# Optimization experiments

Hardware: AMD Instinct MI355X
Metric: run time of the kernel (lower is better)

The kernel has to match this reference:

```python
import jax, jax.numpy as jnp
import numpy as np

N = 32768   # nodes
E = 131072  # directed edges
B = 8       # graphs in batch
F_IN = 1025
NEG = -1e30
EPS = 1e-5


def _lin_init(k, i, o):
    k1, k2 = jax.random.split(k)
    s = 1.0 / np.sqrt(i)
    return (jax.random.uniform(k1, (i, o), jnp.float32, -s, s),
            jax.random.uniform(k2, (o,), jnp.float32, -s, s))


def _bn_init(k, c):
    k1, k2, k3, k4 = jax.random.split(k, 4)
    gamma = jax.random.uniform(k1, (c,), jnp.float32, 0.5, 1.5)
    beta = jax.random.normal(k2, (c,), jnp.float32) * 0.1
    mean = jax.random.normal(k3, (c,), jnp.float32) * 0.1
    var = jax.random.uniform(k4, (c,), jnp.float32, 0.5, 1.5)
    return jnp.stack([gamma, beta, mean, var])  # [4, c]


def setup_inputs() -> dict:
    key = jax.random.key(0)
    ks = jax.random.split(key, 16)
    x = jax.random.normal(ks[0], (N, F_IN), jnp.float32)
    edge_index = jax.random.randint(ks[1], (2, E), 0, N, dtype=jnp.int32)
    batch = jnp.sort(jax.random.randint(ks[2], (N,), 0, B, dtype=jnp.int32))
    pool_w, pool_b = _lin_init(ks[3], 2 * F_IN, 1)
    c1_w0, _ = _lin_init(ks[4], F_IN, 512)
    c1_w1, c1_b = _lin_init(ks[5], F_IN, 512)
    c2_w0, _ = _lin_init(ks[6], 512, 512)
    c2_w1, c2_b = _lin_init(ks[7], 512, 512)
    bn1 = _bn_init(ks[8], 512)
    bn2 = _bn_init(ks[9], 512)
    bn3 = _bn_init(ks[10], 512)
    bn4 = _bn_init(ks[11], 256)
    lin1_w, lin1_b = _lin_init(ks[12], 1024, 512)
    lin2_w, lin2_b = _lin_init(ks[13], 512, 256)
    lin3_w, lin3_b = _lin_init(ks[14], 256, 4)
    return dict(x=x, edge_index=edge_index, batch=batch,
                pool_w=pool_w, pool_b=pool_b,
                c1_w0=c1_w0, c1_w1=c1_w1, c1_b=c1_b,
                c2_w0=c2_w0, c2_w1=c2_w1, c2_b=c2_b,
                bn1=bn1, bn2=bn2, bn3=bn3, bn4=bn4,
                lin1_w=lin1_w, lin1_b=lin1_b,
                lin2_w=lin2_w, lin2_b=lin2_b,
                lin3_w=lin3_w, lin3_b=lin3_b)


def _batchnorm(h, p):
    g, b, m, v = p[0], p[1], p[2], p[3]
    return (h - m) * jax.lax.rsqrt(v + EPS) * g + b


def _cheb(h, row, col, w, w0, w1, b):
    # ChebConv K=2, sym norm, lambda_max=2: out = h@W0 + (L_hat h)@W1 + b,
    # L_hat = -D^{-1/2} A D^{-1/2} (self-loops removed, diag of scaled L is 0)
    deg = jax.ops.segment_sum(w, row, num_segments=N)
    dis = jnp.where(deg > 0, 1.0 / jnp.sqrt(jnp.maximum(deg, 1e-12)), 0.0)
    nrm = -w * dis[row] * dis[col]
    tx1 = jax.ops.segment_sum(nrm[:, None] * h[row], col, num_segments=N)
    return h @ w0 + tx1 @ w1 + b


def _forward(x, edge_index, batch, pool_w, pool_b,
             c1_w0, c1_w1, c1_b, c2_w0, c2_w1, c2_b,
             bn1, bn2, bn3, bn4,
             lin1_w, lin1_b, lin2_w, lin2_b, lin3_w, lin3_b):
    u, v = edge_index[0], edge_index[1]

    # ---- EdgePooling: edge scores = softmax over dst segments, +0.5 ----
    e = (jnp.concatenate([x[u], x[v]], axis=1) @ pool_w + pool_b)[:, 0]  # [E]
    m = jax.ops.segment_max(e, v, num_segments=N)
    ex = jnp.exp(e - m[v])
    score = ex / jax.ops.segment_sum(ex, v, num_segments=N)[v] + 0.5

    # ---- greedy maximal matching in descending score order ----
    order = jnp.argsort(-score)

    def step(used, k):
        uu, vv = u[k], v[k]
        ok = jnp.logical_not(used[uu] | used[vv])
        used = used.at[uu].set(used[uu] | ok)
        used = used.at[vv].set(used[vv] | ok)
        return used, ok

    _, ok_sorted = jax.lax.scan(step, jnp.zeros((N,), bool), order)
    sel = jnp.zeros((E,), bool).at[order].set(ok_sorted)

    rep = jnp.minimum(u, v)  # cluster representative of a merged edge
    cluster = jnp.arange(N, dtype=jnp.int32)
    cluster = cluster.at[jnp.where(sel, u, N)].set(rep, mode='drop')
    cluster = cluster.at[jnp.where(sel, v, N)].set(rep, mode='drop')
    node_score = jnp.ones((N,), x.dtype).at[jnp.where(sel, rep, N)].set(score, mode='drop')
    px = jnp.zeros_like(x).at[cluster].add(x) * node_score[:, None]  # pooled node feats
    valid = cluster == jnp.arange(N, dtype=jnp.int32)  # surviving cluster rows

    # ---- coarsened edge_index, coalesced (dedup), self-loops dropped ----
    cu, cv = cluster[u], cluster[v]
    nonloop = cu != cv
    key = jnp.where(nonloop, cu * N + cv, N * N + jnp.arange(E, dtype=jnp.int32))
    o2 = jnp.argsort(key)
    sk = key[o2]
    first = jnp.concatenate([jnp.ones((1,), bool), sk[1:] != sk[:-1]])
    keep_sorted = first & (sk < N * N)
    w = jnp.zeros((E,), x.dtype).at[o2].set(keep_sorted.astype(x.dtype))

    # ---- two ChebConv + BN(eval) + ReLU ----
    h = jax.nn.relu(_batchnorm(_cheb(px, cu, cv, w, c1_w0, c1_w1, c1_b), bn1))
    h = jax.nn.relu(_batchnorm(_cheb(h, cu, cv, w, c2_w0, c2_w1, c2_b), bn2))

    # ---- global max + mean pool over valid nodes per graph ----
    hmax = jax.ops.segment_max(jnp.where(valid[:, None], h, NEG), batch, num_segments=B)
    cnt = jax.ops.segment_sum(valid.astype(h.dtype), batch, num_segments=B)
    hmean = jax.ops.segment_sum(jnp.where(valid[:, None], h, 0.0), batch,
                                num_segments=B) / jnp.maximum(cnt, 1.0)[:, None]
    g = jnp.concatenate([hmax, hmean], axis=1)  # [B, 1024]

    # ---- readout MLP (dropout off in eval) ----
    g = jax.nn.relu(_batchnorm(g @ lin1_w + lin1_b, bn3))
    g = jax.nn.relu(_batchnorm(g @ lin2_w + lin2_b, bn4))
    feature = g
    out = jax.nn.log_softmax(jax.nn.relu(g @ lin3_w + lin3_b), axis=-1)
    return out, feature


def reference(x, edge_index, batch, pool_w, pool_b,
              c1_w0, c1_w1, c1_b, c2_w0, c2_w1, c2_b,
              bn1, bn2, bn3, bn4,
              lin1_w, lin1_b, lin2_w, lin2_b, lin3_w, lin3_b):
    return _forward(x, edge_index, batch, pool_w, pool_b,
                    c1_w0, c1_w1, c1_b, c2_w0, c2_w1, c2_b,
                    bn1, bn2, bn3, bn4,
                    lin1_w, lin1_b, lin2_w, lin2_b, lin3_w, lin3_b)
```

## Files before the change

kernel.cpp:

```cpp
#include <hip/hip_runtime.h>
#include <hip/hip_bf16.h>
#include <cstdint>
#include <cmath>

typedef unsigned int u32;
typedef unsigned long long u64;
typedef float f32x4 __attribute__((ext_vector_type(4)));
typedef __bf16 bf16x8 __attribute__((ext_vector_type(8)));
typedef unsigned short us8 __attribute__((ext_vector_type(8)));
typedef unsigned short us4 __attribute__((ext_vector_type(4)));

#define NN 32768
#define NE 131072
#define FIN 1025
#define HTS 262144
#define HTM (HTS - 1)

#define WS_A_D    0ul
#define WS_B_D    262144ul
#define WS_EMAX   524288ul
#define WS_SSUM   655360ul
#define WS_EXD    917504ul
#define WS_CIN    917504ul
#define WS_KEY    1966080ul
#define WS_BEST   3014656ul
#define WS_USED   3276800ul
#define WS_CUR    3276800ul
#define WS_ACT0   3407872ul
#define WS_ACT1   3932160ul
#define WS_BTHI   0ul
#define WS_BT2    3407872ul
#define WS_HT     1966080ul
#define WS_RACC1  2097152ul
#define WS_RACC2  2113536ul
#define WS_CIDX   2129920ul
#define WS_PERM   2260992ul
#define WS_BSUM   2392064ul
#define WS_BOFF   2393088ul
#define WS_SCORE  4456448ul
#define WS_CSRA   4456448ul
#define WS_SEL    4980736ul
#define WS_CSRC   4980736ul
#define WS_CLUST  5505024ul
#define WS_OTHER  5636096ul
#define WS_NSC    5767168ul
#define WS_CEU    5898240ul
#define WS_CEV    6422528ul
#define WS_DEG    6946816ul
#define WS_OFF    6946816ul
#define WS_DIS    7077888ul
#define WS_PXL    7077888ul
#define WS_MISC   7208960ul
#define WS_GMAX   7209216ul
#define WS_GSUM   7225600ul
#define WS_GCNT   7241984ul
#define WS_P      7242240ul
#define WS_PB     74351104ul
#define WS_H      141459968ul

__device__ __forceinline__ u32 enc_f(float f) {
    u32 b = __float_as_uint(f);
    return (b & 0x80000000u) ? ~b : (b | 0x80000000u);
}
__device__ __forceinline__ float dec_f(u32 m) {
    return (m & 0x80000000u) ? __uint_as_float(m ^ 0x80000000u) : __uint_as_float(~m);
}
__device__ __forceinline__ double wave_sum(double v) {
    #pragma unroll
    for (int off = 32; off > 0; off >>= 1) v += __shfl_down(v, off, 64);
    return v;
}
__device__ __forceinline__ unsigned short f2bf(float v) {
    u32 b = __float_as_uint(v);
    u32 r = b + 0x7FFFu + ((b >> 16) & 1u);
    return (unsigned short)(r >> 16);
}
__device__ __forceinline__ float bf2f(unsigned short h) {
    return __uint_as_float(((u32)h) << 16);
}
__device__ __forceinline__ bf16x8 ld_frag(const unsigned short* p) {
    union { us8 u; bf16x8 b; } t;
    t.u = *(const us8*)p;
    return t.b;
}
__device__ __forceinline__ void dma16(unsigned short* lds, const unsigned short* g) {
    __builtin_amdgcn_global_load_lds((const __attribute__((address_space(1))) u32*)g,
                                     (__attribute__((address_space(3))) u32*)lds, 16, 0, 0);
}

__global__ void node_dots(const float* __restrict__ x, const float* __restrict__ pw,
                          double* a_d, double* b_d,
                          u32* emax, double* ssum, u32* deg, int* misc,
                          u32* gmaxb, float* gsum, float* gcnt,
                          u64* best, u32* used, int* clus, int* other, float* nsc) {
    int gid = blockIdx.x * blockDim.x + threadIdx.x;
    if (gid < NN) {
        emax[gid] = 0u; ssum[gid] = 0.0; deg[gid] = 0u;
        best[gid] = ~0ull; used[gid] = 0u;
        clus[gid] = gid; other[gid] = -1; nsc[gid] = 1.0f;
    }
    if (gid < 4096) { gmaxb[gid] = 0u; gsum[gid] = 0.0f; }
    if (gid < 64) { misc[gid] = (gid == 1) ? NE : 0; gcnt[gid] = 0.0f; }

    int wave = gid >> 6;
    int lane = threadIdx.x & 63;
    if (wave >= NN) return;
    const float* xr = x + (size_t)wave * FIN;
    double s0 = 0.0, s1 = 0.0;
    for (int f = lane; f < FIN; f += 64) {
        double xv = (double)xr[f];
        s0 += xv * (double)pw[f];
        s1 += xv * (double)pw[FIN + f];
    }
    s0 = wave_sum(s0); s1 = wave_sum(s1);
    if (lane == 0) { a_d[wave] = s0; b_d[wave] = s1; }
}

__global__ void edge_p1(const int* __restrict__ ei, const double* __restrict__ a_d,
                        const double* __restrict__ b_d, const float* __restrict__ pb,
                        double* e_d, u32* emax) {
    int k = blockIdx.x * 256 + threadIdx.x;
    if (k >= NE) return;
    int u = ei[k], v = ei[NE + k];
    double e = a_d[u] + b_d[v] + (double)pb[0];
    e_d[k] = e;
    atomicMax(&emax[v], enc_f((float)e));
}
__global__ void edge_p2(const int* __restrict__ ei, double* e_d,
                        const u32* __restrict__ emax, double* ssum) {
    int k = blockIdx.x * 256 + threadIdx.x;
    if (k >= NE) return;
    int v = ei[NE + k];
    float mf = dec_f(emax[v]);
    double ex = exp(e_d[k] - (double)mf);
    e_d[k] = ex;
    unsafeAtomicAdd(&ssum[v], ex);
}
__global__ void edge_p3(const int* __restrict__ ei, const double* __restrict__ e_d,
                        const double* __restrict__ ssum, float* score, u64* key,
                        int* sel, int* act0, u64* best) {
    int k = blockIdx.x * 256 + threadIdx.x;
    if (k >= NE) return;
    int u = ei[k], v = ei[NE + k];
    float sc = (float)(e_d[k] / ssum[v] + 0.5);
    score[k] = sc;
    u32 m = enc_f(sc);
    u64 kk = ((u64)(m ^ 0xFFFFFFFFu) << 32) | (u32)k;
    key[k] = kk;
    sel[k] = 0;
    act0[k] = k;
    atomicMin(&best[u], kk);
    atomicMin(&best[v], kk);
}

__global__ void mk_sel(const u64* __restrict__ key, const int* __restrict__ ei,
                       const int* __restrict__ act, const int* __restrict__ cntp,
                       int* ncntp, const u64* __restrict__ best,
                       u32* used, int* sel) {
    int cnt = cntp[0];
    int stride = gridDim.x * blockDim.x;
    int gid = blockIdx.x * blockDim.x + threadIdx.x;
    if (gid == 0) ncntp[0] = 0;
    for (int i = gid; i < cnt; i += stride) {
        int e = act[i];
        u64 k = key[e];
        int a = ei[e], b = ei[NE + e];
        if (best[a] == k && best[b] == k) { sel[e] = 1; used[a] = 1u; used[b] = 1u; }
    }
}
__global__ void mk_compact(const int* __restrict__ ei, const int* __restrict__ act,
                           const int* __restrict__ cntp, int* nxt, int* ncntp,
                           u64* best, const u32* __restrict__ used) {
    int cnt = cntp[0];
    int stride = gridDim.x * blockDim.x;
    for (int i = blockIdx.x * blockDim.x + threadIdx.x; i < cnt; i += stride) {
        int e = act[i];
        int a = ei[e], b = ei[NE + e];
        best[a] = ~0ull; best[b] = ~0ull;
        bool live = !(used[a] | used[b]);
        u64 mask = __ballot(live);
        if (mask) {
            int lane = threadIdx.x & 63;
            int leader = __ffsll((unsigned long long)mask) - 1;
            int base = 0;
            if (lane == leader) base = atomicAdd(ncntp, __popcll(mask));
            base = __shfl(base, leader, 64);
            if (live) nxt[base + __popcll(mask & ((1ull << lane) - 1ull))] = e;
        }
    }
}
__global__ void mk_min(const u64* __restrict__ key, const int* __restrict__ ei,
                       const int* __restrict__ act, const int* __restrict__ cntp,
                       u64* best) {
    int cnt = cntp[0];
    int stride = gridDim.x * blockDim.x;
    for (int i = blockIdx.x * blockDim.x + threadIdx.x; i < cnt; i += stride) {
        int e = act[i];
        u64 k = key[e];
        atomicMin(&best[ei[e]], k);
        atomicMin(&best[ei[NE + e]], k);
    }
}
__global__ void __launch_bounds__(1024) match_fin(
        const u64* __restrict__ key, const int* __restrict__ ei,
        int* sel, u64* best, u32* used,
        int* listA, int* listB, const int* __restrict__ cntp) {
    int tid = threadIdx.x;
    int cnt = cntp[0];
    int* cur = listA; int* nxt = listB;
    __shared__ int s_n;
    for (int round = 0; round < 4096 && cnt > 0; ++round) {
        for (int i = tid; i < cnt; i += 1024) {
            int e = cur[i]; u64 k = key[e];
            atomicMin(&best[ei[e]], k);
            atomicMin(&best[ei[NE + e]], k);
        }
        __syncthreads();
        for (int i = tid; i < cnt; i += 1024) {
            int e = cur[i]; u64 k = key[e];
            int a = ei[e], b = ei[NE + e];
            if (best[a] == k && best[b] == k) { sel[e] = 1; used[a] = 1u; used[b] = 1u; }
        }
        if (tid == 0) s_n = 0;
        __syncthreads();
        for (int i = tid; i < cnt; i += 1024) {
            int e = cur[i];
            int a = ei[e], b = ei[NE + e];
            best[a] = ~0ull; best[b] = ~0ull;
            if (!(used[a] | used[b])) {
                int idx = atomicAdd(&s_n, 1);
                nxt[idx] = e;
            }
        }
        __syncthreads();
        cnt = s_n;
        int* t = cur; cur = nxt; nxt = t;
        __syncthreads();
    }
}

__global__ void apply_sel(const int* __restrict__ ei, const int* __restrict__ sel,
                          const float* __restrict__ score,
                          int* cluster, int* other, float* nscore,
                          u32* ht, u32* cin) {
    int e = blockIdx.x * 256 + threadIdx.x;
    ht[e << 1] = 0xFFFFFFFFu;
    ht[(e << 1) + 1] = 0xFFFFFFFFu;
    if (e < NN) cin[e] = 0u;
    if (sel[e] != 1) return;
    int u = ei[e], v = ei[NE + e];
    int rep = min(u, v);
    cluster[u] = rep; cluster[v] = rep;
    if (u != v) other[rep] = u + v - rep;
    nscore[rep] = score[e];
}

__global__ void coarse_build(const int* __restrict__ ei, const int* __restrict__ cluster,
                             u32* ht, int* misc, int* ce_u, int* ce_v, u32* deg,
                             u32* cin) {
    int e = blockIdx.x * 256 + threadIdx.x;
    if (e >= NE) return;
    int cu = cluster[ei[e]], cv = cluster[ei[NE + e]];
    if (cu == cv) return;
    u32 k = (u32)cu * 32768u + (u32)cv;
    u32 h = ((k * 2654435761u) >> 12) & HTM;
    while (true) {
        u32 old = atomicCAS(&ht[h], 0xFFFFFFFFu, k);
        if (old == 0xFFFFFFFFu) {
            int idx = atomicAdd(&misc[0], 1);
            ce_u[idx] = cu; ce_v[idx] = cv;
            atomicAdd(&deg[cu], 1u);
            atomicAdd(&cin[cv], 1u);
            break;
        }
        if (old == k) break;
        h = (h + 1) & HTM;
    }
}
__global__ void dis_kernel(const u32* __restrict__ deg, float* dis,
                           float* racc1, float* racc2,
                           const int* __restrict__ clus, const int* __restrict__ batch,
                           float* gcnt) {
    int n = blockIdx.x * 256 + threadIdx.x;
    if (n >= NN) return;
    u32 d = deg[n];
    dis[n] = d ? (float)(1.0 / sqrt((double)d)) : 0.0f;
    if (n < 4096) racc1[n] = 0.0f;
    if (n < 2048) racc2[n] = 0.0f;
    bool val = (clus[n] == n);
    int bt = batch[n];
    int lane = threadIdx.x & 63;
    #pragma unroll
    for (int g = 0; g < 8; ++g) {
        u64 m = __ballot(val && bt == g);
        if (m && lane == (__ffsll((unsigned long long)m) - 1))
            unsafeAtomicAdd(&gcnt[g], (float)__popcll(m));
    }
}

__global__ void __launch_bounds__(256) scan_part(const u32* __restrict__ cin,
                                                 const int* __restrict__ clus,
                                                 int* __restrict__ bsum) {
    int t = threadIdx.x;
    int i = blockIdx.x * 256 + t;
    int vc = (int)cin[i];
    int vv = (clus[i] == i) ? 1 : 0;
    #pragma unroll
    for (int off = 32; off > 0; off >>= 1) {
        vc += __shfl_down(vc, off, 64);
        vv += __shfl_down(vv, off, 64);
    }
    __shared__ int sc[4], sv[4];
    if ((t & 63) == 0) { sc[t >> 6] = vc; sv[t >> 6] = vv; }
    __syncthreads();
    if (t == 0) {
        bsum[blockIdx.x] = sc[0] + sc[1] + sc[2] + sc[3];
        bsum[128 + blockIdx.x] = sv[0] + sv[1] + sv[2] + sv[3];
    }
}
__global__ void __launch_bounds__(128) scan_mid(const int* __restrict__ bsum,
                                                int* __restrict__ boff, int* misc) {
    __shared__ int s[256];
    int t = threadIdx.x;
    int v0 = bsum[t], v1 = bsum[128 + t];
    s[t] = v0; s[128 + t] = v1;
    __syncthreads();
    for (int d = 1; d < 128; d <<= 1) {
        int a = (t >= d) ? s[t - d] : 0;
        int b = (t >= d) ? s[128 + t - d] : 0;
        __syncthreads();
        if (t >= d) { s[t] += a; s[128 + t] += b; }
        __syncthreads();
    }
    boff[t] = s[t] - v0;
    boff[128 + t] = s[128 + t] - v1;
    if (t == 127) misc[4] = s[255];
}
__global__ void __launch_bounds__(256) scan_fin(const u32* __restrict__ cin,
                                                const int* __restrict__ clus,
                                                const int* __restrict__ boff,
                                                int* off, int* cur, int* cidx, int* perm) {
    __shared__ int s[256];
    int t = threadIdx.x;
    int i = blockIdx.x * 256 + t;
    int vc = (int)cin[i];
    int vv = (clus[i] == i) ? 1 : 0;
    int p = (vc << 9) | vv;
    s[t] = p;
    __syncthreads();
    for (int d = 1; d < 256; d <<= 1) {
        int a = (t >= d) ? s[t - d] : 0;
        __syncthreads();
        if (t >= d) s[t] += a;
        __syncthreads();
    }
    int ex = s[t] - p;
    int o = boff[blockIdx.x] + (ex >> 9);
    off[i] = o; cur[i] = o;
    int c = boff[128 + blockIdx.x] + (ex & 511);
    cidx[i] = c;
    if (vv) perm[c] = i;
}

__global__ void csr_scatter(const int* __restrict__ ce_u, const int* __restrict__ ce_v,
                            const float* __restrict__ dis, const int* __restrict__ misc,
                            int* cur, int* csr_a, float* csr_c,
                            const int* __restrict__ cidx) {
    int e = blockIdx.x * 256 + threadIdx.x;
    if (e >= misc[0]) return;
    int a = ce_u[e], b = ce_v[e];
    int pos = atomicAdd(&cur[b], 1);
    csr_a[pos] = cidx[a];
    csr_c[pos] = -dis[a] * dis[b];
}

__device__ __forceinline__ size_t pk_idx(int r, int k, int KT) {
    return ((((size_t)(r >> 4) * KT + (k >> 5)) << 6) + (((k >> 3) & 3) << 4) + (r & 15)) << 3;
}

__global__ void __launch_bounds__(256) conv_all(
        const float* __restrict__ x, const int* __restrict__ perm,
        const int* __restrict__ misc,
        const int* __restrict__ other, const float* __restrict__ nsc,
        unsigned short* __restrict__ Abf, float* __restrict__ pxl,
        const float* __restrict__ B10, const float* __restrict__ B11,
        unsigned short* __restrict__ Bp1,
        const float* __restrict__ B20, const float* __restrict__ B21,
        unsigned short* __restrict__ Bp2) {
    int bid = blockIdx.x;
    int t = threadIdx.x;
    if (bid < 2048) {
        __shared__ unsigned short S[16][1032];
        __shared__ int Srow[16], So[16];
        __shared__ float Ss[16];
        int cnt = misc[4];
        int tile = bid;
        if ((tile << 4) >= ((cnt + 127) & ~127)) return;
        if (t < 16) {
            int ci = (tile << 4) + t;
            bool val = ci < cnt;
            int row = val ? perm[ci] : -1;
            Srow[t] = row;
            So[t] = val ? other[row] : -1;
            Ss[t] = val ? nsc[row] : 0.0f;
        }
        __syncthreads();
        if (t < 16) {
            int row = Srow[t];
            float v = 0.0f;
            if (row >= 0) {
                int o = So[t];
                v = x[(size_t)row * FIN + 1024];
                if (o >= 0) v += x[(size_t)o * FIN + 1024];
                v *= Ss[t];
            }
            pxl[(tile << 4) + t] = v;
        }
        for (int r = 0; r < 16; ++r) {
            int row = Srow[r];
            int o = So[r];
            float s = Ss[r];
            if (row >= 0) {
                const float* xr = x + (size_t)row * FIN;
                const float* xo = x + (size_t)(o >= 0 ? o : row) * FIN;
                #pragma unroll
                for (int k = 0; k < 4; ++k) {
                    int c = (k << 8) + t;
                    float v = xr[c];
                    if (o >= 0) v += xo[c];
                    S[r][c] = f2bf(v * s);
                }
            } else {
                #pragma unroll
                for (int k = 0; k < 4; ++k) S[r][(k << 8) + t] = 0;
            }
        }
        __syncthreads();
        int wave = t >> 6, lane = t & 63;
        int l16 = lane & 15, quad = lane >> 4;
        #pragma unroll
        for (int kt0 = 0; kt0 < 8; ++kt0) {
            int kt = (kt0 << 2) + wave;
            int c0 = (kt << 5) + (quad << 3);
            us8 v = *(const us8*)&S[l16][c0];
            *(us8*)&Abf[((((size_t)tile << 5) + kt) << 9) + ((size_t)lane << 3)] = v;
        }
    } else if (bid < 2560) {
        int j = bid - 2048;
        int n = ((j & 3) << 8) + t;
        int k0 = (j >> 2) << 3;
        unsigned short h[8];
        #pragma unroll
        for (int jj = 0; jj < 8; ++jj) {
            int k = k0 + jj;
            float v = (n < 512) ? B10[(size_t)k * 512 + n] : B11[(size_t)k * 512 + (n - 512)];
            h[jj] = f2bf(v);
        }
        *(us8*)&Bp1[pk_idx(n, k0, 32)] = *(const us8*)h;
    } else {
        int j = bid - 2560;
        int n = ((j & 3) << 8) + t;
        int k0 = (j >> 2) << 3;
        unsigned short h[8];
        #pragma unroll
        for (int jj = 0; jj < 8; ++jj) {
            int k = k0 + jj;
            float v = (n < 512) ? B20[(size_t)k * 512 + n] : B21[(size_t)k * 512 + (n - 512)];
            h[jj] = f2bf(v);
        }
        *(us8*)&Bp2[pk_idx(n, k0, 16)] = *(const us8*)h;
    }
}

template <bool R1>
__global__ void __launch_bounds__(256, 4) gemm_pk(
        const unsigned short* __restrict__ Ap, const unsigned short* __restrict__ Bp,
        float* __restrict__ P, unsigned short* __restrict__ Pb, int KT,
        const float* __restrict__ pxl, const float* __restrict__ w0,
        const float* __restrict__ w1, const int* __restrict__ msc) {
    __shared__ unsigned short L[2][8192];
    int tid = threadIdx.x;
    int bid = blockIdx.x;
    int loc = bid >> 3;
    int bn = (loc & 7) << 7;
    int bm = ((((bid & 7) << 5) | (loc >> 3))) << 7;
    if (bm >= ((msc[4] + 127) & ~127)) return;
    int wave = tid >> 6, lane = tid & 63, quad = lane >> 4, l16 = lane & 15;
    int moff = (wave >> 1) << 6, noff = (wave & 1) << 6;
    f32x4 acc[4][4];
    #pragma unroll
    for (int i = 0; i < 4; ++i)
        #pragma unroll
        for (int j = 0; j < 4; ++j) acc[i][j] = (f32x4){0.f, 0.f, 0.f, 0.f};

    const unsigned short* src[4];
    unsigned short* dst[4];
    #pragma unroll
    for (int q = 0; q < 4; ++q) {
        int f = (wave << 2) + q;
        int tg = (f < 8) ? ((bm >> 4) + f) : ((bn >> 4) + (f - 8));
        src[q] = ((f < 8) ? Ap : Bp) + (((size_t)tg * KT) << 9) + ((size_t)lane << 3);
        dst[q] = &L[0][(size_t)f << 9];
    }
    const unsigned short* ra = &L[0][(size_t)(wave >> 1) << 11];
    const unsigned short* rb = &L[0][4096 + ((size_t)(wave & 1) << 11)];

    #pragma unroll
    for (int q = 0; q < 4; ++q) dma16(dst[q], src[q]);
    __syncthreads();

    int cur = 0;
    for (int kt = 0; kt < KT; ++kt) {
        if (kt + 1 < KT) {
            int nb = (cur ^ 1) * 8192;
            size_t go = ((size_t)(kt + 1)) << 9;
            #pragma unroll
            for (int q = 0; q < 4; ++q) dma16(dst[q] + nb, src[q] + go);
        }
        const unsigned short* la = ra + cur * 8192;
        const unsigned short* lb = rb + cur * 8192;
        bf16x8 af[4], bf[4];
        #pragma unroll
        for (int i = 0; i < 4; ++i) {
            af[i] = ld_frag(la + ((size_t)i << 9) + (lane << 3));
            bf[i] = ld_frag(lb + ((size_t)i << 9) + (lane << 3));
        }
        #pragma unroll
        for (int mi = 0; mi < 4; ++mi)
            #pragma unroll
            for (int ni = 0; ni < 4; ++ni)
                acc[mi][ni] = __builtin_amdgcn_mfma_f32_16x16x32_bf16(af[mi], bf[ni], acc[mi][ni], 0, 0, 0);
        __syncthreads();
        cur ^= 1;
    }
    #pragma unroll
    for (int mi = 0; mi < 4; ++mi)
        #pragma unroll
        for (int ni = 0; ni < 4; ++ni) {
            int col = bn + noff + (ni << 4) + l16;
            float wl = 0.0f;
            if (R1) wl = (col < 512) ? w0[524288 + col] : w1[524288 + col - 512];
            #pragma unroll
            for (int r2 = 0; r2 < 4; ++r2) {
                int row = bm + moff + (mi << 4) + (quad << 2) + r2;
                float v = acc[mi][ni][r2];
                if (R1) v += pxl[row] * wl;
                if (col < 512) P[(size_t)row * 512 + col] = v;
                else Pb[(size_t)row * 512 + (col - 512)] = f2bf(v);
            }
        }
}

template <bool BF16OUT>
__global__ void __launch_bounds__(256) cheb_fuse(
        const float* __restrict__ P, const unsigned short* __restrict__ Pb,
        const int* __restrict__ off,
        const int* __restrict__ csr_a, const float* __restrict__ csr_c,
        const int* __restrict__ misc, const float* __restrict__ bias,
        const float* __restrict__ bn, float* __restrict__ Hf,
        unsigned short* __restrict__ Hb, const int* __restrict__ perm) {
    int b = (blockIdx.x * 256 + threadIdx.x) >> 6;
    int lane = threadIdx.x & 63;
    if (b >= misc[4]) return;
    int r = perm[b];
    int s = off[r];
    int e = (r < NN - 1) ? off[r + 1] : misc[0];
    int c0 = lane << 3;
    float a0[4], a1[4];
    {
        float4 t0 = *(const float4*)&P[(size_t)b * 512 + c0];
        float4 t1 = *(const float4*)&P[(size_t)b * 512 + c0 + 4];
        a0[0] = t0.x; a0[1] = t0.y; a0[2] = t0.z; a0[3] = t0.w;
        a1[0] = t1.x; a1[1] = t1.y; a1[2] = t1.z; a1[3] = t1.w;
    }
    for (int j = s; j < e; ++j) {
        int a = csr_a[j];
        float cf = csr_c[j];
        us8 raw = *(const us8*)&Pb[(size_t)a * 512 + c0];
        a0[0] = fmaf(cf, bf2f(raw[0]), a0[0]); a0[1] = fmaf(cf, bf2f(raw[1]), a0[1]);
        a0[2] = fmaf(cf, bf2f(raw[2]), a0[2]); a0[3] = fmaf(cf, bf2f(raw[3]), a0[3]);
        a1[0] = fmaf(cf, bf2f(raw[4]), a1[0]); a1[1] = fmaf(cf, bf2f(raw[5]), a1[1]);
        a1[2] = fmaf(cf, bf2f(raw[6]), a1[2]); a1[3] = fmaf(cf, bf2f(raw[7]), a1[3]);
    }
    float o[8];
    #pragma unroll
    for (int i = 0; i < 8; ++i) {
        int j = c0 + i;
        float acc = (i < 4) ? a0[i] : a1[i - 4];
        float ga = bn[j], be = bn[512 + j], mn = bn[1024 + j], vr = bn[1536 + j];
        float sc = (float)(1.0 / sqrt((double)vr + 1e-5));
        float v = (acc + bias[j] - mn) * sc * ga + be;
        o[i] = v > 0.0f ? v : 0.0f;
    }
    if (BF16OUT) {
        unsigned short h[8];
        #pragma unroll
        for (int i = 0; i < 8; ++i) h[i] = f2bf(o[i]);
        *(us8*)&Hb[pk_idx(b, c0, 16)] = *(const us8*)h;
    } else {
        *(float4*)&Hf[(size_t)b * 512 + c0] = make_float4(o[0], o[1], o[2], o[3]);
        *(float4*)&Hf[(size_t)b * 512 + c0 + 4] = make_float4(o[4], o[5], o[6], o[7]);
    }
}

__global__ void __launch_bounds__(256) pool_kernel(
        const float* __restrict__ H, const int* __restrict__ cluster,
        const int* __restrict__ batch, u32* gmaxb, float* gsum,
        const int* __restrict__ cidx) {
    int t = threadIdx.x;
    int n0 = blockIdx.x * 64;
    float m0 = 0.0f, m1 = 0.0f, s0 = 0.0f, s1 = 0.0f;
    int cur = batch[n0];
    for (int i = 0; i < 64; ++i) {
        int n = n0 + i;
        int bt = batch[n];
        if (bt != cur) {
            atomicMax(&gmaxb[cur * 512 + t], __float_as_uint(m0));
            atomicMax(&gmaxb[cur * 512 + t + 256], __float_as_uint(m1));
            unsafeAtomicAdd(&gsum[cur * 512 + t], s0);
            unsafeAtomicAdd(&gsum[cur * 512 + t + 256], s1);
            m0 = m1 = s0 = s1 = 0.0f; cur = bt;
        }
        if (cluster[n] == n) {
            size_t ci = (size_t)cidx[n];
            float h0 = H[ci * 512 + t];
            float h1 = H[ci * 512 + t + 256];
            m0 = fmaxf(m0, h0); m1 = fmaxf(m1, h1);
            s0 += h0; s1 += h1;
        }
    }
    atomicMax(&gmaxb[cur * 512 + t], __float_as_uint(m0));
    atomicMax(&gmaxb[cur * 512 + t + 256], __float_as_uint(m1));
    unsafeAtomicAdd(&gsum[cur * 512 + t], s0);
    unsafeAtomicAdd(&gsum[cur * 512 + t + 256], s1);
}

__global__ void __launch_bounds__(512) ro1(
        const u32* __restrict__ gmaxb, const float* __restrict__ gsum,
        const float* __restrict__ gcnt, const float* __restrict__ l1w,
        float* __restrict__ racc1) {
    int o = threadIdx.x;
    int k0 = blockIdx.x << 4;
    float acc[8] = {0, 0, 0, 0, 0, 0, 0, 0};
    float inv[8];
    #pragma unroll
    for (int b = 0; b < 8; ++b) inv[b] = 1.0f / fmaxf(gcnt[b], 1.0f);
    for (int kk = 0; kk < 16; ++kk) {
        int k = k0 + kk;
        float w = l1w[(size_t)k * 512 + o];
        #pragma unroll
        for (int b = 0; b < 8; ++b) {
            float g = (k < 512) ? __uint_as_float(gmaxb[b * 512 + k])
                                : gsum[b * 512 + (k - 512)] * inv[b];
            acc[b] = fmaf(g, w, acc[b]);
        }
    }
    #pragma unroll
    for (int b = 0; b < 8; ++b) unsafeAtomicAdd(&racc1[b * 512 + o], acc[b]);
}
__global__ void __launch_bounds__(256) ro3(
        const float* __restrict__ racc1, const float* __restrict__ l1b,
        const float* __restrict__ bn3, const float* __restrict__ l2w,
        float* __restrict__ racc2) {
    int o = threadIdx.x;
    int k0 = blockIdx.x << 4;
    float acc[8] = {0, 0, 0, 0, 0, 0, 0, 0};
    for (int kk = 0; kk < 16; ++kk) {
        int k = k0 + kk;
        float ga = bn3[k], be = bn3[512 + k], mn = bn3[1024 + k], vr = bn3[1536 + k];
        float sc = (float)(1.0 / sqrt((double)vr + 1e-5));
        float bi = l1b[k];
        float w = l2w[(size_t)k * 256 + o];
        #pragma unroll
        for (int b = 0; b < 8; ++b) {
            float g1 = (racc1[b * 512 + k] + bi - mn) * sc * ga + be;
            g1 = g1 > 0.0f ? g1 : 0.0f;
            acc[b] = fmaf(g1, w, acc[b]);
        }
    }
    #pragma unroll
    for (int b = 0; b < 8; ++b) unsafeAtomicAdd(&racc2[b * 256 + o], acc[b]);
}
__global__ void __launch_bounds__(256) ro4(
        const float* __restrict__ racc2, const float* __restrict__ l2b,
        const float* __restrict__ bn4, const float* __restrict__ l3w,
        const float* __restrict__ l3b, float* __restrict__ out) {
    __shared__ float G2[8 * 256];
    int o = threadIdx.x;
    {
        float ga = bn4[o], be = bn4[256 + o], mn = bn4[512 + o], vr = bn4[768 + o];
        float sc = (float)(1.0 / sqrt((double)vr + 1e-5));
        float bi = l2b[o];
        #pragma unroll
        for (int b = 0; b < 8; ++b) {
            float v = (racc2[b * 256 + o] + bi - mn) * sc * ga + be;
            v = v > 0.0f ? v : 0.0f;
            G2[b * 256 + o] = v;
            out[32 + b * 256 + o] = v;
        }
    }
    __syncthreads();
    if (o < 8) {
        int b = o;
        float r[4];
        #pragma unroll
        for (int c = 0; c < 4; ++c) {
            float acc = l3b[c];
            for (int k = 0; k < 256; ++k) acc += G2[b * 256 + k] * l3w[k * 4 + c];
            r[c] = acc > 0.0f ? acc : 0.0f;
        }
        float mx = fmaxf(fmaxf(r[0], r[1]), fmaxf(r[2], r[3]));
        float s = 0.0f;
        #pragma unroll
        for (int c = 0; c < 4; ++c) s += expf(r[c] - mx);
        float lse = mx + logf(s);
        #pragma unroll
        for (int c = 0; c < 4; ++c) out[b * 4 + c] = r[c] - lse;
    }
}

extern "C" void kernel_launch(void* const* d_in, const int* in_sizes, int n_in,
                              void* d_out, int out_size, void* d_ws, size_t ws_size,
                              hipStream_t stream) {
    const float* x      = (const float*)d_in[0];
    const int*   ei     = (const int*)d_in[1];
    const int*   batch  = (const int*)d_in[2];
    const float* pool_w = (const float*)d_in[3];
    const float* pool_b = (const float*)d_in[4];
    const float* c1_w0  = (const float*)d_in[5];
    const float* c1_w1  = (const float*)d_in[6];
    const float* c1_b   = (const float*)d_in[7];
    const float* c2_w0  = (const float*)d_in[8];
    const float* c2_w1  = (const float*)d_in[9];
    const float* c2_b   = (const float*)d_in[10];
    const float* bn1    = (const float*)d_in[11];
    const float* bn2    = (const float*)d_in[12];
    const float* bn3    = (const float*)d_in[13];
    const float* bn4    = (const float*)d_in[14];
    const float* l1w    = (const float*)d_in[15];
    const float* l1b    = (const float*)d_in[16];
    const float* l2w    = (const float*)d_in[17];
    const float* l2b    = (const float*)d_in[18];
    const float* l3w    = (const float*)d_in[19];
    const float* l3b    = (const float*)d_in[20];
    float* out = (float*)d_out;
    char* ws = (char*)d_ws;

    double* a_d   = (double*)(ws + WS_A_D);
    double* b_d   = (double*)(ws + WS_B_D);
    u32*    emax  = (u32*)(ws + WS_EMAX);
    double* ssum  = (double*)(ws + WS_SSUM);
    double* exd   = (double*)(ws + WS_EXD);
    u32*    cin   = (u32*)(ws + WS_CIN);
    int*    cidxp = (int*)(ws + WS_CIDX);
    int*    permp = (int*)(ws + WS_PERM);
    int*    bsum  = (int*)(ws + WS_BSUM);
    int*    boffp = (int*)(ws + WS_BOFF);
    u64*    key   = (u64*)(ws + WS_KEY);
    u64*    best  = (u64*)(ws + WS_BEST);
    u32*    used  = (u32*)(ws + WS_USED);
    int*    curp  = (int*)(ws + WS_CUR);
    int*    act0  = (int*)(ws + WS_ACT0);
    int*    act1  = (int*)(ws + WS_ACT1);
    unsigned short* bthi = (unsigned short*)(ws + WS_BTHI);
    unsigned short* bt2  = (unsigned short*)(ws + WS_BT2);
    float*  pxl   = (float*)(ws + WS_PXL);
    u32*    ht    = (u32*)(ws + WS_HT);
    float*  racc1 = (float*)(ws + WS_RACC1);
    float*  racc2 = (float*)(ws + WS_RACC2);
    float*  score = (float*)(ws + WS_SCORE);
    int*    csr_a = (int*)(ws + WS_CSRA);
    int*    sel   = (int*)(ws + WS_SEL);
    float*  csr_c = (float*)(ws + WS_CSRC);
    int*    clus  = (int*)(ws + WS_CLUST);
    int*    other = (int*)(ws + WS_OTHER);
    float*  nsc   = (float*)(ws + WS_NSC);
    int*    ce_u  = (int*)(ws + WS_CEU);
    int*    ce_v  = (int*)(ws + WS_CEV);
    u32*    deg   = (u32*)(ws + WS_DEG);
    int*    off   = (int*)(ws + WS_OFF);
    float*  dis   = (float*)(ws + WS_DIS);
    int*    misc  = (int*)(ws + WS_MISC);
    u32*    gmaxb = (u32*)(ws + WS_GMAX);
    float*  gsum  = (float*)(ws + WS_GSUM);
    float*  gcnt  = (float*)(ws + WS_GCNT);
    float*  P     = (float*)(ws + WS_P);
    unsigned short* Pb = (unsigned short*)(ws + WS_PB);
    unsigned short* ax = (unsigned short*)(ws + WS_H);
    unsigned short* hb = (unsigned short*)(ws + WS_H);
    float*  H     = (float*)(ws + WS_H);

    node_dots<<<NN / 4, 256, 0, stream>>>(x, pool_w, a_d, b_d,
                                          emax, ssum, deg, misc, gmaxb, gsum, gcnt,
                                          best, used, clus, other, nsc);
    edge_p1<<<NE / 256, 256, 0, stream>>>(ei, a_d, b_d, pool_b, exd, emax);
    edge_p2<<<NE / 256, 256, 0, stream>>>(ei, exd, emax, ssum);
    edge_p3<<<NE / 256, 256, 0, stream>>>(ei, exd, ssum, score, key, sel, act0, best);

    {
        static const int gr[9] = {512, 512, 256, 128, 64, 32, 16, 8, 8};
        int* acts[2] = {act0, act1};
        for (int r = 0; r < 8; ++r) {
            int c = r & 1, n = 1 - c;
            mk_sel<<<gr[r], 256, 0, stream>>>(key, ei, acts[c], &misc[1 + c],
                                              &misc[1 + n], best, used, sel);
            mk_compact<<<gr[r], 256, 0, stream>>>(ei, acts[c], &misc[1 + c],
                                                  acts[n], &misc[1 + n], best, used);
            mk_min<<<gr[r + 1], 256, 0, stream>>>(key, ei, acts[n], &misc[1 + n], best);
        }
        match_fin<<<1, 1024, 0, stream>>>(key, ei, sel, best, used,
                                          act0, act1, &misc[1]);
    }

    apply_sel<<<NE / 256, 256, 0, stream>>>(ei, sel, score, clus, other, nsc, ht, cin);
    coarse_build<<<NE / 256, 256, 0, stream>>>(ei, clus, ht, misc, ce_u, ce_v, deg, cin);
    dis_kernel<<<NN / 256, 256, 0, stream>>>(deg, dis, racc1, racc2, clus, batch, gcnt);
    scan_part<<<128, 256, 0, stream>>>(cin, clus, bsum);
    scan_mid<<<1, 128, 0, stream>>>(bsum, boffp, misc);
    scan_fin<<<128, 256, 0, stream>>>(cin, clus, boffp, off, curp, cidxp, permp);
    csr_scatter<<<NE / 256, 256, 0, stream>>>(ce_u, ce_v, dis, misc, curp, csr_a, csr_c,
                                              cidxp);

    conv_all<<<2816, 256, 0, stream>>>(x, permp, misc, other, nsc, ax, pxl,
                                       c1_w0, c1_w1, bthi, c2_w0, c2_w1, bt2);
    gemm_pk<true><<<2048, 256, 0, stream>>>(ax, bthi, P, Pb, 32, pxl, c1_w0, c1_w1, misc);
    cheb_fuse<true><<<NN / 4, 256, 0, stream>>>(P, Pb, off, csr_a, csr_c, misc, c1_b, bn1,
                                                nullptr, hb, permp);

    gemm_pk<false><<<2048, 256, 0, stream>>>(hb, bt2, P, Pb, 16, nullptr, nullptr, nullptr,
                                             misc);
    cheb_fuse<false><<<NN / 4, 256, 0, stream>>>(P, Pb, off, csr_a, csr_c, misc, c2_b, bn2,
                                                 H, nullptr, permp);

    pool_kernel<<<NN / 64, 256, 0, stream>>>(H, clus, batch, gmaxb, gsum, cidxp);

    ro1<<<64, 512, 0, stream>>>(gmaxb, gsum, gcnt, l1w, racc1);
    ro3<<<32, 256, 0, stream>>>(racc1, l1b, bn3, l2w, racc2);
    ro4<<<1, 256, 0, stream>>>(racc2, l2b, bn4, l3w, l3b, out);
}
```

Baseline: 732.4 us.

## Transpose GEMM MFMA operands for vectorized epilogue stores and shrink pool blocks

The GEMM swaps the MFMA operand order so each lane holds four consecutive output columns of one row. This lets the epilogue write float4 and 4-wide bf16 vectors instead of scattered scalar stores, and load the rank-1 weight correction as a float4. The block-index swizzle is dropped in favour of a plain row-major tile order, which may change L2 reuse. The pool kernel now processes 16 nodes per block instead of 64, giving more blocks but more atomics.

Measured after the change: 720.0 us. About the same (-1.7%).

```diff
diff --git a/kernel.cpp b/kernel.cpp
--- a/kernel.cpp
+++ b/kernel.cpp
@@ -481,9 +481,8 @@
     __shared__ unsigned short L[2][8192];
     int tid = threadIdx.x;
     int bid = blockIdx.x;
-    int loc = bid >> 3;
-    int bn = (loc & 7) << 7;
-    int bm = ((((bid & 7) << 5) | (loc >> 3))) << 7;
+    int bn = (bid & 7) << 7;
+    int bm = (bid >> 3) << 7;
     if (bm >= ((msc[4] + 127) & ~127)) return;
     int wave = tid >> 6, lane = tid & 63, quad = lane >> 4, l16 = lane & 15;
     int moff = (wave >> 1) << 6, noff = (wave & 1) << 6;
@@ -526,29 +525,39 @@
             bf[i] = ld_frag(lb + ((size_t)i << 9) + (lane << 3));
         }
         #pragma unroll
-        for (int mi = 0; mi < 4; ++mi)
+        for (int ni = 0; ni < 4; ++ni)
             #pragma unroll
-            for (int ni = 0; ni < 4; ++ni)
-                acc[mi][ni] = __builtin_amdgcn_mfma_f32_16x16x32_bf16(af[mi], bf[ni], acc[mi][ni], 0, 0, 0);
+            for (int mi = 0; mi < 4; ++mi)
+                acc[ni][mi] = __builtin_amdgcn_mfma_f32_16x16x32_bf16(bf[ni], af[mi], acc[ni][mi], 0, 0, 0);
         __syncthreads();
         cur ^= 1;
     }
     #pragma unroll
-    for (int mi = 0; mi < 4; ++mi)
+    for (int mi = 0; mi < 4; ++mi) {
+        int m = bm + moff + (mi << 4) + l16;
+        float pm = 0.0f;
+        if (R1) pm = pxl[m];
         #pragma unroll
         for (int ni = 0; ni < 4; ++ni) {
-            int col = bn + noff + (ni << 4) + l16;
-            float wl = 0.0f;
-            if (R1) wl = (col < 512) ? w0[524288 + col] : w1[524288 + col - 512];
-            #pragma unroll
-            for (int r2 = 0; r2 < 4; ++r2) {
-                int row = bm + moff + (mi << 4) + (quad << 2) + r2;
-                float v = acc[mi][ni][r2];
-                if (R1) v += pxl[row] * wl;
-                if (col < 512) P[(size_t)row * 512 + col] = v;
-                else Pb[(size_t)row * 512 + (col - 512)] = f2bf(v);
+            int n0 = bn + noff + (ni << 4) + (quad << 2);
+            float v0 = acc[ni][mi][0], v1 = acc[ni][mi][1];
+            float v2 = acc[ni][mi][2], v3 = acc[ni][mi][3];
+            if (bn < 512) {
+                if (R1) {
+                    float4 wv = *(const float4*)&w0[524288 + n0];
+                    v0 += pm * wv.x; v1 += pm * wv.y; v2 += pm * wv.z; v3 += pm * wv.w;
+                }
+                *(float4*)&P[(size_t)m * 512 + n0] = make_float4(v0, v1, v2, v3);
+            } else {
+                if (R1) {
+                    float4 wv = *(const float4*)&w1[524288 + n0 - 512];
+                    v0 += pm * wv.x; v1 += pm * wv.y; v2 += pm * wv.z; v3 += pm * wv.w;
+                }
+                unsigned short h[4] = {f2bf(v0), f2bf(v1), f2bf(v2), f2bf(v3)};
+                *(us4*)&Pb[(size_t)m * 512 + (n0 - 512)] = *(const us4*)h;
             }
         }
+    }
 }
 
 template <bool BF16OUT>
@@ -608,10 +617,10 @@
         const int* __restrict__ batch, u32* gmaxb, float* gsum,
         const int* __restrict__ cidx) {
     int t = threadIdx.x;
-    int n0 = blockIdx.x * 64;
+    int n0 = blockIdx.x * 16;
     float m0 = 0.0f, m1 = 0.0f, s0 = 0.0f, s1 = 0.0f;
     int cur = batch[n0];
-    for (int i = 0; i < 64; ++i) {
+    for (int i = 0; i < 16; ++i) {
         int n = n0 + i;
         int bt = batch[n];
         if (bt != cur) {
@@ -832,7 +841,7 @@
     cheb_fuse<false><<<NN / 4, 256, 0, stream>>>(P, Pb, off, csr_a, csr_c, misc, c2_b, bn2,
                                                  H, nullptr, permp);
 
-    pool_kernel<<<NN / 64, 256, 0, stream>>>(H, clus, batch, gmaxb, gsum, cidxp);
+    pool_kernel<<<NN / 16, 256, 0, stream>>>(H, clus, batch, gmaxb, gsum, cidxp);
 
     ro1<<<64, 512, 0, stream>>>(gmaxb, gsum, gcnt, l1w, racc1);
     ro3<<<32, 256, 0, stream>>>(racc1, l1b, bn3, l2w, racc2);
```
